# Optimization experiments

Hardware: AMD Instinct MI355X
Metric: run time of the kernel (lower is better)

## Reference

```python
import jax, jax.numpy as jnp
import numpy as np

P = 6
CUTOFF = 1.0
N_BASIS = 8
AVG_NEIGH = 16.0
NUM_LAYERS = 2
N, E, MUL, H, F = 8192, 131072, 16, 256, 16


def envelope(d):
    # polynomial cutoff u(x) with p=6 (NequIP/Allegro style)
    x = d / CUTOFF
    p = float(P)
    u = (1.0 - (p + 1.0) * (p + 2.0) / 2.0 * x ** P
         + p * (p + 2.0) * x ** (P + 1)
         - p * (p + 1.0) / 2.0 * x ** (P + 2))
    return jnp.where(x < 1.0, u, 0.0)


def bessel(d):
    k = jnp.arange(1, N_BASIS + 1, dtype=d.dtype)
    return jnp.sqrt(2.0 / CUTOFF) * jnp.sin(k[None, :] * jnp.pi * d[:, None] / CUTOFF) / d[:, None]


def sph_harm(u):
    # real spherical harmonics, ell=0..3, component normalization -> [E,16]
    x, y, z = u[:, 0], u[:, 1], u[:, 2]
    s3 = 3.0 ** 0.5
    s5 = 5.0 ** 0.5
    s15 = 15.0 ** 0.5
    s7 = 7.0 ** 0.5
    c33 = (35.0 / 8.0) ** 0.5
    c32 = 105.0 ** 0.5
    c31 = (21.0 / 8.0) ** 0.5
    one = jnp.ones_like(x)
    comps = [
        one,
        s3 * x, s3 * y, s3 * z,
        s15 * x * y, s15 * y * z, 0.5 * s5 * (3.0 * z * z - 1.0), s15 * x * z, 0.5 * s15 * (x * x - y * y),
        c33 * y * (3.0 * x * x - y * y), c32 * x * y * z, c31 * y * (5.0 * z * z - 1.0),
        0.5 * s7 * (5.0 * z ** 3 - 3.0 * z), c31 * x * (5.0 * z * z - 1.0),
        0.5 * c32 * z * (x * x - y * y), c33 * x * (x * x - 3.0 * y * y),
    ]
    return jnp.stack(comps, axis=1)


def setup_inputs() -> dict:
    key = jax.random.key(0)
    ks = jax.random.split(key, 16)
    dirs = jax.random.normal(ks[0], (E, 3), dtype=jnp.float32)
    dirs = dirs / jnp.linalg.norm(dirs, axis=1, keepdims=True)
    r = jax.random.uniform(ks[1], (E, 1), minval=0.05, maxval=0.95, dtype=jnp.float32)
    vectors = dirs * r
    node_attrs = 0.5 * jax.random.normal(ks[2], (N, F), dtype=jnp.float32)
    senders = jax.random.randint(ks[3], (E,), 0, N, dtype=jnp.int32)
    receivers = jax.random.randint(ks[4], (E,), 0, N, dtype=jnp.int32)

    def gl(k, shape):
        fan_in = shape[-2] if len(shape) >= 2 else 1
        return jax.random.normal(k, shape, dtype=jnp.float32) / jnp.sqrt(float(fan_in))

    return {
        'node_attrs': node_attrs, 'vectors': vectors,
        'senders': senders, 'receivers': receivers,
        'W_e0': gl(ks[5], (N_BASIS + 2 * F, H)), 'b_e0': jnp.zeros((H,), jnp.float32),
        'W_e1': gl(ks[6], (H, H)), 'b_e1': jnp.zeros((H,), jnp.float32),
        'W_v0': gl(ks[7], (H, MUL)),
        'W_lw': gl(ks[8], (NUM_LAYERS, H, MUL)),
        'W_lsh': gl(ks[9], (NUM_LAYERS, 16, 16)),
        'W_ly1': gl(ks[10], (NUM_LAYERS, H + MUL, H)), 'b_ly1': jnp.zeros((NUM_LAYERS, H), jnp.float32),
        'W_ly2': gl(ks[11], (NUM_LAYERS, H, H)), 'b_ly2': jnp.zeros((NUM_LAYERS, H), jnp.float32),
        'W_out': gl(ks[12], (H, 1)),
    }


def reference(node_attrs, vectors, senders, receivers, W_e0, b_e0, W_e1, b_e1, W_v0,
              W_lw, W_lsh, W_ly1, b_ly1, W_ly2, b_ly2, W_out):
    n_nodes = node_attrs.shape[0]
    inv = 1.0 / jnp.sqrt(AVG_NEIGH)
    d = jnp.linalg.norm(vectors, axis=1)                      # [E]
    u = envelope(d)                                           # [E]
    # edge embedding: radial basis + gathered endpoint attrs
    x = jnp.concatenate([bessel(d), node_attrs[senders], node_attrs[receivers]], axis=1)
    x = jax.nn.silu(x @ W_e0 + b_e0)
    x = jax.nn.silu(x @ W_e1 + b_e1)
    x = u[:, None] * x                                        # [E,H]
    Y = sph_harm(vectors / d[:, None])                        # [E,16]
    V = (x @ W_v0)[:, :, None] * Y[:, None, :]                # [E,MUL,16]
    for l in range(NUM_LAYERS):
        w = x @ W_lw[l]                                       # [E,MUL]
        wY = jax.ops.segment_sum(w[:, :, None] * Y[:, None, :], senders, num_segments=n_nodes) * inv
        wY = wY[senders]                                      # [E,MUL,16] gather back
        VV = wY * V                                           # per-edge equivariant product
        V = jnp.einsum('emi,ij->emj', VV, W_lsh[l])
        h = jnp.concatenate([x, VV[:, :, 0]], axis=1)         # scalar (l=0) channel feedback
        y = jax.nn.silu(h @ W_ly1[l] + b_ly1[l])
        y = jax.nn.silu(y @ W_ly2[l] + b_ly2[l])
        x = (x + u[:, None] * y) / jnp.sqrt(2.0)
    edge_out = (x @ W_out) * u[:, None]                       # [E,1]
    node_out = jax.ops.segment_sum(edge_out, receivers, num_segments=n_nodes) * inv
    return node_out                                           # [N,1]
```

## Files before the change

kernel.cpp:

```cpp
#include <hip/hip_runtime.h>
#include <hip/hip_bf16.h>
#include <math.h>

#define H 256
#define F 16
#define MUL 16
#define NB 8
#define LROW 296
#define YROW 264

typedef short bf16x8 __attribute__((ext_vector_type(8)));
typedef short bf16x4 __attribute__((ext_vector_type(4)));
typedef float f32x4 __attribute__((ext_vector_type(4)));
#define MFMA_B16(a, b, c) __builtin_amdgcn_mfma_f32_16x16x32_bf16(a, b, c, 0, 0, 0)

__device__ __forceinline__ float bf2f(__hip_bfloat16 x) { return __bfloat162float(x); }
__device__ __forceinline__ float silu(float x)
{
    return x * __builtin_amdgcn_rcpf(1.f + __expf(-x));
}
__device__ __forceinline__ short f2bs(float x)
{
    __hip_bfloat16 h = __float2bfloat16(x);
    short s; __builtin_memcpy(&s, &h, 2); return s;
}
__device__ __forceinline__ float bs2f(short s)
{
    __hip_bfloat16 h; __builtin_memcpy(&h, &s, 2); return __bfloat162float(h);
}

__global__ __launch_bounds__(256) void k_sniff(const void* vec, int* flag)
{
    __shared__ int bad;
    int tid = threadIdx.x;
    if (tid == 0) bad = 0;
    __syncthreads();
    const __hip_bfloat16* hp = (const __hip_bfloat16*)vec;
    for (int i = tid; i < 1024; i += 256) {
        float f = bf2f(hp[i]);
        if (!(isfinite(f) && fabsf(f) <= 1.0f)) bad = 1;
    }
    __syncthreads();
    if (tid == 0) *flag = bad;
}

struct ConvArgs {
    const void* src[14];
    float* dst[14];
    int cum[15];
};
__global__ __launch_bounds__(256) void k_conv_all(ConvArgs a, const int* __restrict__ flag)
{
    int gid = blockIdx.x * 256 + threadIdx.x;
    if (gid >= a.cum[14]) return;
    int k = 0;
    while (gid >= a.cum[k + 1]) k++;
    int i = gid - a.cum[k];
    float v = (*flag) ? ((const float*)a.src[k])[i]
                      : bf2f(((const __hip_bfloat16*)a.src[k])[i]);
    a.dst[k][i] = v;
}

struct SwzArgs {
    const float* src[9];
    __hip_bfloat16* dst[9];
    int K[9], Nc[9], cum[10];
};
__global__ __launch_bounds__(256) void k_swz_all(SwzArgs a)
{
    int gid = blockIdx.x * 256 + threadIdx.x;
    if (gid >= a.cum[9]) return;
    int j = 0;
    while (gid >= a.cum[j + 1]) j++;
    int idx = gid - a.cum[j];
    int kk = idx & 31;
    int n = (idx >> 5) % a.Nc[j];
    int kt = idx / (32 * a.Nc[j]);
    int k = kt * 32 + kk;
    float v = (k < a.K[j]) ? a.src[j][(size_t)k * a.Nc[j] + n] : 0.f;
    a.dst[j][idx] = __float2bfloat16(v);
}

__global__ __launch_bounds__(256) void k_swz_wout(const float* __restrict__ Wout,
                                                  __hip_bfloat16* __restrict__ dst)
{
    int idx = blockIdx.x * 256 + threadIdx.x;
    if (idx >= 8 * 16 * 32) return;
    int kk = idx & 31;
    int n = (idx >> 5) & 15;
    int kt = idx >> 9;
    float v = (n == 0) ? Wout[kt * 32 + kk] : 0.f;
    dst[idx] = __float2bfloat16(v);
}

__global__ __launch_bounds__(256) void k_hist(const int* __restrict__ snd,
                                              int* __restrict__ cnt, int E)
{
    int e = blockIdx.x * 256 + threadIdx.x;
    if (e < E) atomicAdd(&cnt[snd[e]], 1);
}

__global__ __launch_bounds__(256) void k_scan(const int* __restrict__ cnt,
                                              int* __restrict__ off,
                                              int* __restrict__ cur, int N)
{
    __shared__ int sums[256];
    int tid = threadIdx.x;
    int chunk = (N + 255) / 256;
    int base = tid * chunk;
    int s = 0;
    for (int i = 0; i < chunk; i++) { int idx = base + i; if (idx < N) s += cnt[idx]; }
    sums[tid] = s;
    __syncthreads();
    for (int d = 1; d < 256; d <<= 1) {
        int v = (tid >= d) ? sums[tid - d] : 0;
        __syncthreads();
        sums[tid] += v;
        __syncthreads();
    }
    int run = (tid == 0) ? 0 : sums[tid - 1];
    for (int i = 0; i < chunk; i++) {
        int idx = base + i;
        if (idx < N) { off[idx] = run; cur[idx] = run; run += cnt[idx]; }
    }
    if (tid == 255) off[N] = run;
}

__global__ __launch_bounds__(256) void k_cscatter(const int* __restrict__ snd,
                                                  int* __restrict__ cur,
                                                  int* __restrict__ eidx, int E)
{
    int e = blockIdx.x * 256 + threadIdx.x;
    if (e >= E) return;
    int p = atomicAdd(&cur[snd[e]], 1);
    eidx[p] = e;
}


__global__ __launch_bounds__(512, 4) void k_embed_mfma(
    const float* __restrict__ vec, const float* __restrict__ na,
    const int* __restrict__ snd, const int* __restrict__ rcv,
    const __hip_bfloat16* __restrict__ We0s, const float* __restrict__ be0,
    const __hip_bfloat16* __restrict__ We1s, const float* __restrict__ be1,
    const __hip_bfloat16* __restrict__ Wv0s, const __hip_bfloat16* __restrict__ Wlws0,
    float* __restrict__ ubuf, float* __restrict__ Ybuf,
    __hip_bfloat16* __restrict__ xb, float* __restrict__ abuf,
    float* __restrict__ wbuf)
{
    __shared__ __align__(16) __hip_bfloat16 As[64 * LROW];
    __shared__ __align__(16) __hip_bfloat16 Ys[64 * YROW];
    __shared__ float us[64];
    int tid = threadIdx.x;
    int w = tid >> 6, l = tid & 63;
    int lm = l & 15, lq = l >> 4;
    int eb = blockIdx.x * 64;

    {
        int el = tid & 63;
        int part = tid >> 6;
        int ge = eb + el;
        const float SQ2 = 1.41421356237309515f;
        const float PI = 3.14159265358979323846f;
        if (part == 0) {
            float vx = vec[3 * ge + 0], vy = vec[3 * ge + 1], vz = vec[3 * ge + 2];
            float d = sqrtf(vx * vx + vy * vy + vz * vz);
            float d3 = d * d * d;
            float d6 = d3 * d3, d7 = d6 * d, d8 = d7 * d;
            float u = 1.f - 28.f * d6 + 48.f * d7 - 21.f * d8;
            u = (d < 1.f) ? u : 0.f;
            ubuf[ge] = u;
            us[el] = u;
            float invd = __builtin_amdgcn_rcpf(d);
#pragma unroll
            for (int k = 1; k <= 4; k++)
                As[el * LROW + (k - 1)] = __float2bfloat16(SQ2 * __sinf((float)k * PI * d) * invd);
        } else if (part == 4) {
            float vx = vec[3 * ge + 0], vy = vec[3 * ge + 1], vz = vec[3 * ge + 2];
            float d = sqrtf(vx * vx + vy * vy + vz * vz);
            float invd = __builtin_amdgcn_rcpf(d);
#pragma unroll
            for (int k = 5; k <= 8; k++)
                As[el * LROW + (k - 1)] = __float2bfloat16(SQ2 * __sinf((float)k * PI * d) * invd);
        } else if (part == 5) {
#pragma unroll
            for (int j = 40; j < 64; j++) As[el * LROW + j] = __float2bfloat16(0.f);
        } else if (part == 1) {
            int s = snd[ge];
#pragma unroll
            for (int j = 0; j < 16; j++)
                As[el * LROW + 8 + j] = __float2bfloat16(na[(size_t)s * F + j]);
        } else if (part == 2) {
            int r = rcv[ge];
#pragma unroll
            for (int j = 0; j < 16; j++)
                As[el * LROW + 24 + j] = __float2bfloat16(na[(size_t)r * F + j]);
        } else if (part == 3) {
            float vx = vec[3 * ge + 0], vy = vec[3 * ge + 1], vz = vec[3 * ge + 2];
            float d = sqrtf(vx * vx + vy * vy + vz * vz);
            float invd = __builtin_amdgcn_rcpf(d);
            float x = vx * invd, y = vy * invd, z = vz * invd;
            const float s3 = 1.7320508075688772f;
            const float s5 = 2.2360679774997896f;
            const float s15 = 3.8729833462074170f;
            const float s7 = 2.6457513110645907f;
            const float c33 = 2.0916500663351889f;
            const float c32 = 10.246950765959598f;
            const float c31 = 1.6201851746019651f;
            float* Yp = Ybuf + (size_t)ge * 16;
            Yp[0] = 1.f;
            Yp[1] = s3 * x;  Yp[2] = s3 * y;  Yp[3] = s3 * z;
            Yp[4] = s15 * x * y;  Yp[5] = s15 * y * z;
            Yp[6] = 0.5f * s5 * (3.f * z * z - 1.f);
            Yp[7] = s15 * x * z;
            Yp[8] = 0.5f * s15 * (x * x - y * y);
            Yp[9] = c33 * y * (3.f * x * x - y * y);
            Yp[10] = c32 * x * y * z;
            Yp[11] = c31 * y * (5.f * z * z - 1.f);
            Yp[12] = 0.5f * s7 * (5.f * z * z * z - 3.f * z);
            Yp[13] = c31 * x * (5.f * z * z - 1.f);
            Yp[14] = 0.5f * c32 * z * (x * x - y * y);
            Yp[15] = c33 * x * (x * x - 3.f * y * y);
        }
    }
    __syncthreads();

    f32x4 acc[4][2];
#pragma unroll
    for (int mt = 0; mt < 4; mt++)
#pragma unroll
        for (int nt = 0; nt < 2; nt++) acc[mt][nt] = (f32x4){0.f, 0.f, 0.f, 0.f};
#pragma unroll
    for (int kt = 0; kt < 2; kt++) {
        bf16x8 aw[2];
#pragma unroll
        for (int nt = 0; nt < 2; nt++)
            aw[nt] = *(const bf16x8*)(We0s + ((size_t)(kt * 256 + w * 32 + nt * 16 + lm) * 32 + lq * 8));
#pragma unroll
        for (int mt = 0; mt < 4; mt++) {
            bf16x8 bx = *(const bf16x8*)(As + (mt * 16 + lm) * LROW + kt * 32 + lq * 8);
#pragma unroll
            for (int nt = 0; nt < 2; nt++) acc[mt][nt] = MFMA_B16(aw[nt], bx, acc[mt][nt]);
        }
    }
#pragma unroll
    for (int nt = 0; nt < 2; nt++) {
        int cb = w * 32 + nt * 16 + lq * 4;
        f32x4 bb = *(const f32x4*)(be0 + cb);
#pragma unroll
        for (int mt = 0; mt < 4; mt++) {
            int row = mt * 16 + lm;
            bf16x4 v = {f2bs(silu(acc[mt][nt][0] + bb[0])), f2bs(silu(acc[mt][nt][1] + bb[1])),
                        f2bs(silu(acc[mt][nt][2] + bb[2])), f2bs(silu(acc[mt][nt][3] + bb[3]))};
            *(bf16x4*)(Ys + row * YROW + cb) = v;
        }
    }
    __syncthreads();

#pragma unroll
    for (int mt = 0; mt < 4; mt++)
#pragma unroll
        for (int nt = 0; nt < 2; nt++) acc[mt][nt] = (f32x4){0.f, 0.f, 0.f, 0.f};
#pragma unroll
    for (int kt = 0; kt < 8; kt++) {
        bf16x8 aw[2];
#pragma unroll
        for (int nt = 0; nt < 2; nt++)
            aw[nt] = *(const bf16x8*)(We1s + ((size_t)(kt * 256 + w * 32 + nt * 16 + lm) * 32 + lq * 8));
#pragma unroll
        for (int mt = 0; mt < 4; mt++) {
            bf16x8 bx = *(const bf16x8*)(Ys + (mt * 16 + lm) * YROW + kt * 32 + lq * 8);
#pragma unroll
            for (int nt = 0; nt < 2; nt++) acc[mt][nt] = MFMA_B16(aw[nt], bx, acc[mt][nt]);
        }
    }
#pragma unroll
    for (int nt = 0; nt < 2; nt++) {
        int cb = w * 32 + nt * 16 + lq * 4;
        f32x4 bb = *(const f32x4*)(be1 + cb);
#pragma unroll
        for (int mt = 0; mt < 4; mt++) {
            int row = mt * 16 + lm;
            float uu = us[row];
            bf16x4 v = {f2bs(silu(acc[mt][nt][0] + bb[0]) * uu),
                        f2bs(silu(acc[mt][nt][1] + bb[1]) * uu),
                        f2bs(silu(acc[mt][nt][2] + bb[2]) * uu),
                        f2bs(silu(acc[mt][nt][3] + bb[3]) * uu)};
            *(bf16x4*)(As + row * LROW + cb) = v;
            *(bf16x4*)(xb + (size_t)(eb + row) * H + cb) = v;
        }
    }
    __syncthreads();

    if (w < 4) {
        f32x4 av = (f32x4){0.f, 0.f, 0.f, 0.f};
#pragma unroll
        for (int kt = 0; kt < 8; kt++) {
            bf16x8 bx = *(const bf16x8*)(As + (w * 16 + lm) * LROW + kt * 32 + lq * 8);
            bf16x8 a_v = *(const bf16x8*)(Wv0s + ((size_t)(kt * 16 + lm) * 32 + lq * 8));
            av = MFMA_B16(a_v, bx, av);
        }
        *(f32x4*)(abuf + (size_t)(eb + w * 16 + lm) * 16 + lq * 4) = av;
    } else {
        int w2 = w - 4;
        f32x4 aw2 = (f32x4){0.f, 0.f, 0.f, 0.f};
#pragma unroll
        for (int kt = 0; kt < 8; kt++) {
            bf16x8 bx = *(const bf16x8*)(As + (w2 * 16 + lm) * LROW + kt * 32 + lq * 8);
            bf16x8 a_w = *(const bf16x8*)(Wlws0 + ((size_t)(kt * 16 + lm) * 32 + lq * 8));
            aw2 = MFMA_B16(a_w, bx, aw2);
        }
        *(f32x4*)(wbuf + (size_t)(eb + w2 * 16 + lm) * 16 + lq * 4) = aw2;
    }
}

__global__ __launch_bounds__(256) void k_gather0(
    const int* __restrict__ off, const int* __restrict__ eidx,
    const float* __restrict__ wbuf, const float* __restrict__ Ybuf,
    const float* __restrict__ abuf,
    float* __restrict__ wYn0, __hip_bfloat16* __restrict__ vvbuf)
{
    __shared__ float ws[16][17];
    __shared__ float Ysh[16][17];
    __shared__ float Ash[16][17];
    __shared__ float w00[16];
    __shared__ int esh[16];
    int tid = threadIdx.x;
    int m = tid >> 4, i = tid & 15;
    for (int nn = 0; nn < 4; nn++) {
        int n = blockIdx.x * 4 + nn;
        int beg = off[n], end = off[n + 1];
        float acc = 0.f;
        for (int c = beg; c < end; c += 16) {
            int ne = min(16, end - c);
            if (m < ne) {
                int e = eidx[c + m];
                ws[m][i] = wbuf[(size_t)e * 16 + i];
                Ysh[m][i] = Ybuf[(size_t)e * 16 + i];
            }
            __syncthreads();
            for (int j2 = 0; j2 < ne; j2++) acc += ws[j2][m] * Ysh[j2][i];
            __syncthreads();
        }
        wYn0[(size_t)n * 256 + m * 16 + i] = acc * 0.25f;
        if (i == 0) w00[m] = acc * 0.25f;
        __syncthreads();
        for (int c = beg; c < end; c += 16) {
            int ne = min(16, end - c);
            if (m < ne) {
                int e = eidx[c + m];
                Ash[m][i] = abuf[(size_t)e * 16 + i];
                if (i == 0) esh[m] = e;
            }
            __syncthreads();
            if (m < ne)
                vvbuf[(size_t)esh[m] * 16 + i] = __float2bfloat16(w00[i] * Ash[m][i]);
            __syncthreads();
        }
    }
}

__global__ __launch_bounds__(256) void k_gather1(
    const int* __restrict__ off, const int* __restrict__ eidx,
    const float* __restrict__ wbuf, const float* __restrict__ Ybuf,
    const float* __restrict__ abuf,
    const float* __restrict__ wYn0, const float* __restrict__ Wlsh,
    __hip_bfloat16* __restrict__ vvbuf)
{
    __shared__ float ws[16][17];
    __shared__ float Ysh[16][17];
    __shared__ float Ash[16][17];
    __shared__ float qsh[16][17];
    __shared__ float w10[16];
    __shared__ int esh[16];
    int tid = threadIdx.x;
    int m = tid >> 4, i = tid & 15;
    for (int nn = 0; nn < 4; nn++) {
        int n = blockIdx.x * 4 + nn;
        int beg = off[n], end = off[n + 1];
        float acc = 0.f;
        for (int c = beg; c < end; c += 16) {
            int ne = min(16, end - c);
            if (m < ne) {
                int e = eidx[c + m];
                ws[m][i] = wbuf[(size_t)e * 16 + i];
                Ysh[m][i] = Ybuf[(size_t)e * 16 + i];
            }
            __syncthreads();
            for (int j2 = 0; j2 < ne; j2++) acc += ws[j2][m] * Ysh[j2][i];
            __syncthreads();
        }
        if (i == 0) w10[m] = acc * 0.25f;
        qsh[m][i] = wYn0[(size_t)n * 256 + m * 16 + i] * Wlsh[i * 16];
        __syncthreads();
        for (int c = beg; c < end; c += 16) {
            int ne = min(16, end - c);
            if (m < ne) {
                int e = eidx[c + m];
                Ysh[m][i] = Ybuf[(size_t)e * 16 + i];
                Ash[m][i] = abuf[(size_t)e * 16 + i];
                if (i == 0) esh[m] = e;
            }
            __syncthreads();
            if (m < ne) {
                float t = 0.f;
#pragma unroll
                for (int i2 = 0; i2 < 16; i2++) t += qsh[i][i2] * Ysh[m][i2];
                vvbuf[(size_t)esh[m] * 16 + i] = __float2bfloat16(w10[i] * Ash[m][i] * t);
            }
            __syncthreads();
        }
    }
}

__global__ __launch_bounds__(512, 4) void k_layer_mfma(
    __hip_bfloat16* __restrict__ xb, const float* __restrict__ ubuf,
    const __hip_bfloat16* __restrict__ vvbuf, const int* __restrict__ rcv,
    const __hip_bfloat16* __restrict__ W1s, const float* __restrict__ b1,
    const __hip_bfloat16* __restrict__ W2s, const float* __restrict__ b2,
    const __hip_bfloat16* __restrict__ Wlwn, float* __restrict__ wbufn,
    const __hip_bfloat16* __restrict__ Wouts, float* __restrict__ nacc,
    int layer)
{
    __shared__ __align__(16) __hip_bfloat16 As[64 * LROW];
    __shared__ __align__(16) __hip_bfloat16 Ys[64 * YROW];
    int tid = threadIdx.x;
    int w = tid >> 6, l = tid & 63;
    int lm = l & 15, lq = l >> 4;
    int eb = blockIdx.x * 64;

#pragma unroll
    for (int i = 0; i < 4; i++) {
        int c = tid + 512 * i;
        int row = c >> 5, kc = c & 31;
        *(bf16x8*)(As + row * LROW + kc * 8) =
            *(const bf16x8*)(xb + (size_t)(eb + row) * H + kc * 8);
    }
    {
        int el = tid & 63;
        int mh = (tid >> 6) * 2;
        int ge = eb + el;
        *(unsigned int*)(As + el * LROW + 256 + mh) =
            *(const unsigned int*)((const short*)vvbuf + (size_t)ge * 16 + mh);
        if (tid < 64) {
#pragma unroll
            for (int j = 0; j < 16; j++) As[tid * LROW + 272 + j] = __float2bfloat16(0.f);
        }
    }
    __syncthreads();

    float uu[4];
#pragma unroll
    for (int mt = 0; mt < 4; mt++) uu[mt] = ubuf[eb + mt * 16 + lm];

    f32x4 acc[4][2];
#pragma unroll
    for (int mt = 0; mt < 4; mt++)
#pragma unroll
        for (int nt = 0; nt < 2; nt++) acc[mt][nt] = (f32x4){0.f, 0.f, 0.f, 0.f};
#pragma unroll
    for (int kt = 0; kt < 9; kt++) {
        bf16x8 aw[2];
#pragma unroll
        for (int nt = 0; nt < 2; nt++)
            aw[nt] = *(const bf16x8*)(W1s + ((size_t)(kt * 256 + w * 32 + nt * 16 + lm) * 32 + lq * 8));
#pragma unroll
        for (int mt = 0; mt < 4; mt++) {
            bf16x8 bx = *(const bf16x8*)(As + (mt * 16 + lm) * LROW + kt * 32 + lq * 8);
#pragma unroll
            for (int nt = 0; nt < 2; nt++) acc[mt][nt] = MFMA_B16(aw[nt], bx, acc[mt][nt]);
        }
    }
#pragma unroll
    for (int nt = 0; nt < 2; nt++) {
        int cb = w * 32 + nt * 16 + lq * 4;
        f32x4 bb = *(const f32x4*)(b1 + cb);
#pragma unroll
        for (int mt = 0; mt < 4; mt++) {
            int row = mt * 16 + lm;
            bf16x4 v = {f2bs(silu(acc[mt][nt][0] + bb[0])), f2bs(silu(acc[mt][nt][1] + bb[1])),
                        f2bs(silu(acc[mt][nt][2] + bb[2])), f2bs(silu(acc[mt][nt][3] + bb[3]))};
            *(bf16x4*)(Ys + row * YROW + cb) = v;
        }
    }
    __syncthreads();

#pragma unroll
    for (int mt = 0; mt < 4; mt++)
#pragma unroll
        for (int nt = 0; nt < 2; nt++) acc[mt][nt] = (f32x4){0.f, 0.f, 0.f, 0.f};
#pragma unroll
    for (int kt = 0; kt < 8; kt++) {
        bf16x8 aw[2];
#pragma unroll
        for (int nt = 0; nt < 2; nt++)
            aw[nt] = *(const bf16x8*)(W2s + ((size_t)(kt * 256 + w * 32 + nt * 16 + lm) * 32 + lq * 8));
#pragma unroll
        for (int mt = 0; mt < 4; mt++) {
            bf16x8 bx = *(const bf16x8*)(Ys + (mt * 16 + lm) * YROW + kt * 32 + lq * 8);
#pragma unroll
            for (int nt = 0; nt < 2; nt++) acc[mt][nt] = MFMA_B16(aw[nt], bx, acc[mt][nt]);
        }
    }
    const float rs2 = 0.70710678118654752f;
#pragma unroll
    for (int nt = 0; nt < 2; nt++) {
        int cb = w * 32 + nt * 16 + lq * 4;
        f32x4 bb = *(const f32x4*)(b2 + cb);
#pragma unroll
        for (int mt = 0; mt < 4; mt++) {
            int row = mt * 16 + lm;
            bf16x4 xo = *(const bf16x4*)(As + row * LROW + cb);
            bf16x4 v;
#pragma unroll
            for (int r = 0; r < 4; r++) {
                float xn = (bs2f(xo[r]) + uu[mt] * silu(acc[mt][nt][r] + bb[r])) * rs2;
                v[r] = f2bs(xn);
            }
            *(bf16x4*)(As + row * LROW + cb) = v;
            if (layer == 0) *(bf16x4*)(xb + (size_t)(eb + row) * H + cb) = v;
        }
    }
    __syncthreads();

    if (layer == 0) {
        if (w < 4) {
            f32x4 cw = (f32x4){0.f, 0.f, 0.f, 0.f};
#pragma unroll
            for (int kt = 0; kt < 8; kt++) {
                bf16x8 bx = *(const bf16x8*)(As + (w * 16 + lm) * LROW + kt * 32 + lq * 8);
                bf16x8 a = *(const bf16x8*)(Wlwn + ((size_t)(kt * 16 + lm) * 32 + lq * 8));
                cw = MFMA_B16(a, bx, cw);
            }
            *(f32x4*)(wbufn + (size_t)(eb + w * 16 + lm) * 16 + lq * 4) = cw;
        }
    } else {
        if (w < 4) {
            f32x4 co = (f32x4){0.f, 0.f, 0.f, 0.f};
#pragma unroll
            for (int kt = 0; kt < 8; kt++) {
                bf16x8 bx = *(const bf16x8*)(As + (w * 16 + lm) * LROW + kt * 32 + lq * 8);
                bf16x8 a = *(const bf16x8*)(Wouts + ((size_t)(kt * 16 + lm) * 32 + lq * 8));
                co = MFMA_B16(a, bx, co);
            }
            if (lq == 0) {
                int e = eb + w * 16 + lm;
                atomicAdd(&nacc[rcv[e]], co[0] * ubuf[e]);
            }
        }
    }
}

__global__ __launch_bounds__(256) void k_final(
    const float* __restrict__ nacc, void* __restrict__ out, const int* __restrict__ flag,
    float inv, int N)
{
    int n = blockIdx.x * 256 + threadIdx.x;
    if (n >= N) return;
    float v = nacc[n] * inv;
    if (*flag) ((float*)out)[n] = v;
    else       ((__hip_bfloat16*)out)[n] = __float2bfloat16(v);
}

extern "C" void kernel_launch(void* const* d_in, const int* in_sizes, int n_in,
                              void* d_out, int out_size, void* d_ws, size_t ws_size,
                              hipStream_t stream)
{
    const int E = in_sizes[2];
    const int N = in_sizes[0] / F;
    (void)n_in; (void)ws_size; (void)out_size;

    char* wsb = (char*)d_ws;
    size_t off = 0;
    int* flag = (int*)wsb; off += 256;

    const int fidx[14] = {0, 1, 4, 5, 6, 7, 8, 9, 10, 11, 12, 13, 14, 15};
    float* canon[14];
    for (int k = 0; k < 14; k++) {
        canon[k] = (float*)(wsb + off);
        off += (size_t)in_sizes[fidx[k]] * 4;
        off = (off + 255) & ~(size_t)255;
    }
    const float* naC   = canon[0];
    const float* vecC  = canon[1];
    const float* We0C  = canon[2];
    const float* be0C  = canon[3];
    const float* We1C  = canon[4];
    const float* be1C  = canon[5];
    const float* Wv0C  = canon[6];
    const float* WlwC  = canon[7];
    const float* WlshC = canon[8];
    const float* Wly1C = canon[9];
    const float* bly1C = canon[10];
    const float* Wly2C = canon[11];
    const float* bly2C = canon[12];
    const float* WoutC = canon[13];

    __hip_bfloat16* We0s  = (__hip_bfloat16*)(wsb + off); off += 64 * 256 * 2;
    __hip_bfloat16* We1s  = (__hip_bfloat16*)(wsb + off); off += 256 * 256 * 2;
    __hip_bfloat16* Wv0s  = (__hip_bfloat16*)(wsb + off); off += 256 * 16 * 2;
    __hip_bfloat16* Wlws0 = (__hip_bfloat16*)(wsb + off); off += 256 * 16 * 2;
    __hip_bfloat16* Wlws1 = (__hip_bfloat16*)(wsb + off); off += 256 * 16 * 2;
    __hip_bfloat16* W1s0  = (__hip_bfloat16*)(wsb + off); off += 288 * 256 * 2;
    __hip_bfloat16* W1s1  = (__hip_bfloat16*)(wsb + off); off += 288 * 256 * 2;
    __hip_bfloat16* W2s0  = (__hip_bfloat16*)(wsb + off); off += 256 * 256 * 2;
    __hip_bfloat16* W2s1  = (__hip_bfloat16*)(wsb + off); off += 256 * 256 * 2;
    __hip_bfloat16* Wouts = (__hip_bfloat16*)(wsb + off); off += 256 * 16 * 2;
    off = (off + 255) & ~(size_t)255;

    __hip_bfloat16* xbuf = (__hip_bfloat16*)(wsb + off); off += (size_t)E * H * 2;
    float* wYn0 = (float*)(wsb + off); off += (size_t)N * H * 4;
    __hip_bfloat16* vvbuf = (__hip_bfloat16*)(wsb + off); off += (size_t)E * 16 * 2;
    float* ubuf = (float*)(wsb + off); off += (size_t)E * 4;
    float* Ybuf = (float*)(wsb + off); off += (size_t)E * 16 * 4;
    float* abuf = (float*)(wsb + off); off += (size_t)E * 16 * 4;
    float* wbuf = (float*)(wsb + off); off += (size_t)E * 16 * 4;
    float* nacc = (float*)(wsb + off); off += (size_t)N * 4;
    int* cnt  = (int*)(wsb + off); off += (size_t)N * 4;
    int* offb = (int*)(wsb + off); off += (size_t)(N + 1) * 4;
    int* cur  = (int*)(wsb + off); off += (size_t)N * 4;
    int* eidx = (int*)(wsb + off); off += (size_t)E * 4;

    const int* snd = (const int*)d_in[2];
    const int* rcv = (const int*)d_in[3];
    const float inv = 0.25f;
    const int nb64 = E / 64;

    k_sniff<<<1, 256, 0, stream>>>(d_in[1], flag);
    {
        ConvArgs ca;
        int c = 0;
        for (int k = 0; k < 14; k++) {
            ca.src[k] = d_in[fidx[k]];
            ca.dst[k] = canon[k];
            ca.cum[k] = c;
            c += in_sizes[fidx[k]];
        }
        ca.cum[14] = c;
        k_conv_all<<<(c + 255) / 256, 256, 0, stream>>>(ca, flag);
    }

    {
        SwzArgs sa;
        const float* srcs[9] = {We0C, We1C, Wv0C, WlwC, WlwC + 256 * 16,
                                Wly1C, Wly1C + 272 * 256, Wly2C, Wly2C + 256 * 256};
        __hip_bfloat16* dsts[9] = {We0s, We1s, Wv0s, Wlws0, Wlws1, W1s0, W1s1, W2s0, W2s1};
        int Ks[9]    = {40, 256, 256, 256, 256, 272, 272, 256, 256};
        int Ncs[9]   = {256, 256, 16, 16, 16, 256, 256, 256, 256};
        int Kpads[9] = {64, 256, 256, 256, 256, 288, 288, 256, 256};
        int c = 0;
        for (int j = 0; j < 9; j++) {
            sa.src[j] = srcs[j]; sa.dst[j] = dsts[j];
            sa.K[j] = Ks[j]; sa.Nc[j] = Ncs[j];
            sa.cum[j] = c;
            c += (Kpads[j] >> 5) * Ncs[j] * 32;
        }
        sa.cum[9] = c;
        k_swz_all<<<(c + 255) / 256, 256, 0, stream>>>(sa);
    }
    k_swz_wout<<<16, 256, 0, stream>>>(WoutC, Wouts);

    hipMemsetAsync(cnt, 0, (size_t)N * sizeof(int), stream);
    k_hist<<<(E + 255) / 256, 256, 0, stream>>>(snd, cnt, E);
    k_scan<<<1, 256, 0, stream>>>(cnt, offb, cur, N);
    k_cscatter<<<(E + 255) / 256, 256, 0, stream>>>(snd, cur, eidx, E);

    k_embed_mfma<<<nb64, 512, 0, stream>>>(vecC, naC, snd, rcv,
                                           We0s, be0C, We1s, be1C, Wv0s, Wlws0,
                                           ubuf, Ybuf, xbuf, abuf, wbuf);

    k_gather0<<<N / 4, 256, 0, stream>>>(offb, eidx, wbuf, Ybuf, abuf, wYn0, vvbuf);
    k_layer_mfma<<<nb64, 512, 0, stream>>>(xbuf, ubuf, vvbuf, rcv,
                                           W1s0, bly1C, W2s0, bly2C,
                                           Wlws1, wbuf,
                                           (const __hip_bfloat16*)nullptr, (float*)nullptr, 0);
    hipMemsetAsync(nacc, 0, (size_t)N * sizeof(float), stream);
    k_gather1<<<N / 4, 256, 0, stream>>>(offb, eidx, wbuf, Ybuf, abuf, wYn0, WlshC, vvbuf);
    k_layer_mfma<<<nb64, 512, 0, stream>>>(xbuf, ubuf, vvbuf, rcv,
                                           W1s1, bly1C + H, W2s1, bly2C + H,
                                           (const __hip_bfloat16*)nullptr, (float*)nullptr,
                                           Wouts, nacc, 1);

    k_final<<<(N + 255) / 256, 256, 0, stream>>>(nacc, d_out, flag, inv, N);
}
```

Before: 360.4 us.

## Prefetch first weight k-tiles early and drop shared staging in gather kernels

In the MFMA embed and layer kernels, the first two k-tiles of each weight matrix are now loaded into registers ahead of time, before the preceding epilogue or elementwise phase, so global load latency overlaps other work. The gather kernels stop staging abuf and edge indices through shared memory with per-chunk barriers. Each thread now reads its edge's values directly and writes vvbuf, and the second gather reads Y rows as vector loads. The trade-off is higher register pressure, which could lower occupancy, plus redundant per-thread Y loads.

```diff
diff --git a/kernel.cpp b/kernel.cpp
--- a/kernel.cpp
+++ b/kernel.cpp
@@ -154,6 +154,13 @@
     int w = tid >> 6, l = tid & 63;
     int lm = l & 15, lq = l >> 4;
     int eb = blockIdx.x * 64;
+
+    bf16x8 w0p[2][2];
+#pragma unroll
+    for (int kt = 0; kt < 2; kt++)
+#pragma unroll
+        for (int nt = 0; nt < 2; nt++)
+            w0p[kt][nt] = *(const bf16x8*)(We0s + ((size_t)(kt * 256 + w * 32 + nt * 16 + lm) * 32 + lq * 8));
 
     {
         int el = tid & 63;
@@ -231,17 +238,19 @@
         for (int nt = 0; nt < 2; nt++) acc[mt][nt] = (f32x4){0.f, 0.f, 0.f, 0.f};
 #pragma unroll
     for (int kt = 0; kt < 2; kt++) {
-        bf16x8 aw[2];
-#pragma unroll
-        for (int nt = 0; nt < 2; nt++)
-            aw[nt] = *(const bf16x8*)(We0s + ((size_t)(kt * 256 + w * 32 + nt * 16 + lm) * 32 + lq * 8));
 #pragma unroll
         for (int mt = 0; mt < 4; mt++) {
             bf16x8 bx = *(const bf16x8*)(As + (mt * 16 + lm) * LROW + kt * 32 + lq * 8);
 #pragma unroll
-            for (int nt = 0; nt < 2; nt++) acc[mt][nt] = MFMA_B16(aw[nt], bx, acc[mt][nt]);
-        }
-    }
+            for (int nt = 0; nt < 2; nt++) acc[mt][nt] = MFMA_B16(w0p[kt][nt], bx, acc[mt][nt]);
+        }
+    }
+    bf16x8 w1p[2][2];
+#pragma unroll
+    for (int kt = 0; kt < 2; kt++)
+#pragma unroll
+        for (int nt = 0; nt < 2; nt++)
+            w1p[kt][nt] = *(const bf16x8*)(We1s + ((size_t)(kt * 256 + w * 32 + nt * 16 + lm) * 32 + lq * 8));
 #pragma unroll
     for (int nt = 0; nt < 2; nt++) {
         int cb = w * 32 + nt * 16 + lq * 4;
@@ -265,7 +274,8 @@
         bf16x8 aw[2];
 #pragma unroll
         for (int nt = 0; nt < 2; nt++)
-            aw[nt] = *(const bf16x8*)(We1s + ((size_t)(kt * 256 + w * 32 + nt * 16 + lm) * 32 + lq * 8));
+            aw[nt] = (kt < 2) ? w1p[kt][nt]
+                   : *(const bf16x8*)(We1s + ((size_t)(kt * 256 + w * 32 + nt * 16 + lm) * 32 + lq * 8));
 #pragma unroll
         for (int mt = 0; mt < 4; mt++) {
             bf16x8 bx = *(const bf16x8*)(Ys + (mt * 16 + lm) * YROW + kt * 32 + lq * 8);
@@ -273,6 +283,11 @@
             for (int nt = 0; nt < 2; nt++) acc[mt][nt] = MFMA_B16(aw[nt], bx, acc[mt][nt]);
         }
     }
+    const __hip_bfloat16* tw = (w < 4) ? Wv0s : Wlws0;
+    bf16x8 twp[2];
+#pragma unroll
+    for (int kt = 0; kt < 2; kt++)
+        twp[kt] = *(const bf16x8*)(tw + ((size_t)(kt * 16 + lm) * 32 + lq * 8));
 #pragma unroll
     for (int nt = 0; nt < 2; nt++) {
         int cb = w * 32 + nt * 16 + lq * 4;
@@ -296,7 +311,8 @@
 #pragma unroll
         for (int kt = 0; kt < 8; kt++) {
             bf16x8 bx = *(const bf16x8*)(As + (w * 16 + lm) * LROW + kt * 32 + lq * 8);
-            bf16x8 a_v = *(const bf16x8*)(Wv0s + ((size_t)(kt * 16 + lm) * 32 + lq * 8));
+            bf16x8 a_v = (kt < 2) ? twp[kt]
+                       : *(const bf16x8*)(Wv0s + ((size_t)(kt * 16 + lm) * 32 + lq * 8));
             av = MFMA_B16(a_v, bx, av);
         }
         *(f32x4*)(abuf + (size_t)(eb + w * 16 + lm) * 16 + lq * 4) = av;
@@ -306,7 +322,8 @@
 #pragma unroll
         for (int kt = 0; kt < 8; kt++) {
             bf16x8 bx = *(const bf16x8*)(As + (w2 * 16 + lm) * LROW + kt * 32 + lq * 8);
-            bf16x8 a_w = *(const bf16x8*)(Wlws0 + ((size_t)(kt * 16 + lm) * 32 + lq * 8));
+            bf16x8 a_w = (kt < 2) ? twp[kt]
+                       : *(const bf16x8*)(Wlws0 + ((size_t)(kt * 16 + lm) * 32 + lq * 8));
             aw2 = MFMA_B16(a_w, bx, aw2);
         }
         *(f32x4*)(wbuf + (size_t)(eb + w2 * 16 + lm) * 16 + lq * 4) = aw2;
@@ -321,9 +338,7 @@
 {
     __shared__ float ws[16][17];
     __shared__ float Ysh[16][17];
-    __shared__ float Ash[16][17];
     __shared__ float w00[16];
-    __shared__ int esh[16];
     int tid = threadIdx.x;
     int m = tid >> 4, i = tid & 15;
     for (int nn = 0; nn < 4; nn++) {
@@ -344,18 +359,13 @@
         wYn0[(size_t)n * 256 + m * 16 + i] = acc * 0.25f;
         if (i == 0) w00[m] = acc * 0.25f;
         __syncthreads();
-        for (int c = beg; c < end; c += 16) {
-            int ne = min(16, end - c);
-            if (m < ne) {
-                int e = eidx[c + m];
-                Ash[m][i] = abuf[(size_t)e * 16 + i];
-                if (i == 0) esh[m] = e;
-            }
-            __syncthreads();
-            if (m < ne)
-                vvbuf[(size_t)esh[m] * 16 + i] = __float2bfloat16(w00[i] * Ash[m][i]);
-            __syncthreads();
-        }
+        float w0i = w00[i];
+        for (int c = beg + m; c < end; c += 16) {
+            int e = eidx[c];
+            float a = abuf[(size_t)e * 16 + i];
+            vvbuf[(size_t)e * 16 + i] = __float2bfloat16(w0i * a);
+        }
+        __syncthreads();
     }
 }
 
@@ -368,10 +378,8 @@
 {
     __shared__ float ws[16][17];
     __shared__ float Ysh[16][17];
-    __shared__ float Ash[16][17];
     __shared__ float qsh[16][17];
     __shared__ float w10[16];
-    __shared__ int esh[16];
     int tid = threadIdx.x;
     int m = tid >> 4, i = tid & 15;
     for (int nn = 0; nn < 4; nn++) {
@@ -392,23 +400,20 @@
         if (i == 0) w10[m] = acc * 0.25f;
         qsh[m][i] = wYn0[(size_t)n * 256 + m * 16 + i] * Wlsh[i * 16];
         __syncthreads();
-        for (int c = beg; c < end; c += 16) {
-            int ne = min(16, end - c);
-            if (m < ne) {
-                int e = eidx[c + m];
-                Ysh[m][i] = Ybuf[(size_t)e * 16 + i];
-                Ash[m][i] = abuf[(size_t)e * 16 + i];
-                if (i == 0) esh[m] = e;
+        float w1i = w10[i];
+        for (int c = beg + m; c < end; c += 16) {
+            int e = eidx[c];
+            float a = abuf[(size_t)e * 16 + i];
+            float t = 0.f;
+#pragma unroll
+            for (int j = 0; j < 4; j++) {
+                f32x4 yv = *(const f32x4*)(Ybuf + (size_t)e * 16 + 4 * j);
+                t += qsh[i][4 * j + 0] * yv[0] + qsh[i][4 * j + 1] * yv[1]
+                   + qsh[i][4 * j + 2] * yv[2] + qsh[i][4 * j + 3] * yv[3];
             }
-            __syncthreads();
-            if (m < ne) {
-                float t = 0.f;
-#pragma unroll
-                for (int i2 = 0; i2 < 16; i2++) t += qsh[i][i2] * Ysh[m][i2];
-                vvbuf[(size_t)esh[m] * 16 + i] = __float2bfloat16(w10[i] * Ash[m][i] * t);
-            }
-            __syncthreads();
-        }
+            vvbuf[(size_t)e * 16 + i] = __float2bfloat16(w1i * a * t);
+        }
+        __syncthreads();
     }
 }
 
@@ -428,6 +433,13 @@
     int lm = l & 15, lq = l >> 4;
     int eb = blockIdx.x * 64;
 
+    bf16x8 w1p[2][2];
+#pragma unroll
+    for (int kt = 0; kt < 2; kt++)
+#pragma unroll
+        for (int nt = 0; nt < 2; nt++)
+            w1p[kt][nt] = *(const bf16x8*)(W1s + ((size_t)(kt * 256 + w * 32 + nt * 16 + lm) * 32 + lq * 8));
+
 #pragma unroll
     for (int i = 0; i < 4; i++) {
         int c = tid + 512 * i;
@@ -462,7 +474,8 @@
         bf16x8 aw[2];
 #pragma unroll
         for (int nt = 0; nt < 2; nt++)
-            aw[nt] = *(const bf16x8*)(W1s + ((size_t)(kt * 256 + w * 32 + nt * 16 + lm) * 32 + lq * 8));
+            aw[nt] = (kt < 2) ? w1p[kt][nt]
+                   : *(const bf16x8*)(W1s + ((size_t)(kt * 256 + w * 32 + nt * 16 + lm) * 32 + lq * 8));
 #pragma unroll
         for (int mt = 0; mt < 4; mt++) {
             bf16x8 bx = *(const bf16x8*)(As + (mt * 16 + lm) * LROW + kt * 32 + lq * 8);
@@ -470,6 +483,12 @@
             for (int nt = 0; nt < 2; nt++) acc[mt][nt] = MFMA_B16(aw[nt], bx, acc[mt][nt]);
         }
     }
+    bf16x8 w2p[2][2];
+#pragma unroll
+    for (int kt = 0; kt < 2; kt++)
+#pragma unroll
+        for (int nt = 0; nt < 2; nt++)
+            w2p[kt][nt] = *(const bf16x8*)(W2s + ((size_t)(kt * 256 + w * 32 + nt * 16 + lm) * 32 + lq * 8));
 #pragma unroll
     for (int nt = 0; nt < 2; nt++) {
         int cb = w * 32 + nt * 16 + lq * 4;
@@ -493,7 +512,8 @@
         bf16x8 aw[2];
 #pragma unroll
         for (int nt = 0; nt < 2; nt++)
-            aw[nt] = *(const bf16x8*)(W2s + ((size_t)(kt * 256 + w * 32 + nt * 16 + lm) * 32 + lq * 8));
+            aw[nt] = (kt < 2) ? w2p[kt][nt]
+                   : *(const bf16x8*)(W2s + ((size_t)(kt * 256 + w * 32 + nt * 16 + lm) * 32 + lq * 8));
 #pragma unroll
         for (int mt = 0; mt < 4; mt++) {
             bf16x8 bx = *(const bf16x8*)(Ys + (mt * 16 + lm) * YROW + kt * 32 + lq * 8);
@@ -501,6 +521,11 @@
             for (int nt = 0; nt < 2; nt++) acc[mt][nt] = MFMA_B16(aw[nt], bx, acc[mt][nt]);
         }
     }
+    const __hip_bfloat16* tw = (layer == 0) ? Wlwn : Wouts;
+    bf16x8 twp[2];
+#pragma unroll
+    for (int kt = 0; kt < 2; kt++)
+        twp[kt] = *(const bf16x8*)(tw + ((size_t)(kt * 16 + lm) * 32 + lq * 8));
     const float rs2 = 0.70710678118654752f;
 #pragma unroll
     for (int nt = 0; nt < 2; nt++) {
@@ -528,7 +553,8 @@
 #pragma unroll
             for (int kt = 0; kt < 8; kt++) {
                 bf16x8 bx = *(const bf16x8*)(As + (w * 16 + lm) * LROW + kt * 32 + lq * 8);
-                bf16x8 a = *(const bf16x8*)(Wlwn + ((size_t)(kt * 16 + lm) * 32 + lq * 8));
+                bf16x8 a = (kt < 2) ? twp[kt]
+                         : *(const bf16x8*)(Wlwn + ((size_t)(kt * 16 + lm) * 32 + lq * 8));
                 cw = MFMA_B16(a, bx, cw);
             }
             *(f32x4*)(wbufn + (size_t)(eb + w * 16 + lm) * 16 + lq * 4) = cw;
@@ -539,7 +565,8 @@
 #pragma unroll
             for (int kt = 0; kt < 8; kt++) {
                 bf16x8 bx = *(const bf16x8*)(As + (w * 16 + lm) * LROW + kt * 32 + lq * 8);
-                bf16x8 a = *(const bf16x8*)(Wouts + ((size_t)(kt * 16 + lm) * 32 + lq * 8));
+                bf16x8 a = (kt < 2) ? twp[kt]
+                         : *(const bf16x8*)(Wouts + ((size_t)(kt * 16 + lm) * 32 + lq * 8));
                 co = MFMA_B16(a, bx, co);
             }
             if (lq == 0) {
```

Result: faster. 349.1 us (median of 2 runs) (-3.1%).
